# Optimization experiments

Measured on AMD Instinct MI355X. Metric: run time of the kernel, lower is better.

The kernel has to match this reference:

```python
import jax, jax.numpy as jnp
import numpy as np


def setup_inputs() -> dict:
    key = jax.random.key(0)
    k1, k2 = jax.random.split(key)
    T, C, H, W = 32, 3, 720, 1280
    x = jax.random.normal(k1, (T, C, H, W), dtype=jnp.float32)
    # flow displacements of a few pixels, realistic optical-flow magnitudes
    flow = jax.random.normal(k2, (T - 2, 2, H, W), dtype=jnp.float32) * 4.0
    return {"x": x, "flow": flow}


def reference(x, flow):
    T, C, H, W = x.shape
    N = T - 2
    # base pixel coordinate grids (computed once, broadcast over frames)
    idx_x = jnp.arange(H, dtype=jnp.float32)[:, None]   # [H,1] -> row coord
    idx_y = jnp.arange(W, dtype=jnp.float32)[None, :]   # [1,W] -> col coord

    fwd = flow[:N]        # flow[t-1] for t=1..N
    bwd = flow[::-1][:N]  # flow[-t]  for t=1..N

    # round+clamp flow-shifted coordinates (jnp.round = round-half-even, matches torch.round)
    ix_f = jnp.clip(jnp.round(idx_x + fwd[:, 0]), 0, H - 1).astype(jnp.int32)  # [N,H,W]
    iy_f = jnp.clip(jnp.round(idx_y + fwd[:, 1]), 0, W - 1).astype(jnp.int32)
    ix_b = jnp.clip(jnp.round(idx_x + bwd[:, 0]), 0, H - 1).astype(jnp.int32)
    iy_b = jnp.clip(jnp.round(idx_y + bwd[:, 1]), 0, W - 1).astype(jnp.int32)

    def gather(frame, ix, iy):  # frame [C,H,W], ix/iy [H,W] -> [C,H,W]
        return frame[:, ix, iy]

    x_fwd = jax.vmap(gather)(x[2:T], ix_f, iy_f)   # warp of x[t+1]
    x_bwd = jax.vmap(gather)(x[0:N], ix_b, iy_b)   # warp of x[t-1]
    xc = x[1:N + 1]                                # center frames x[t]

    # [N, 2C, H, W]
    return jnp.concatenate([xc - x_fwd, xc - x_bwd], axis=1)
```

## Files before the change

kernel.cpp:

```cpp
#include <hip/hip_runtime.h>
#include <hip/hip_bf16.h>


#define TT 32
#define CC 3
#define HH 720
#define WW 1280
#define NN (TT - 2)

__device__ __forceinline__ int clampi(int v, int lo, int hi) {
    return v < lo ? lo : (v > hi ? hi : v);
}

__global__ __launch_bounds__(256) void warp_diff_kernel(
    const float* __restrict__ x,
    const float* __restrict__ flow,
    float* __restrict__ out)
{
    const int WQ = WW / 4;
    int idx = blockIdx.x * blockDim.x + threadIdx.x;
    const int total = NN * HH * WQ;
    if (idx >= total) return;

    int wq = idx % WQ;
    int t  = idx / WQ;
    int h  = t % HH;
    int n  = t / HH;
    int w0 = wq * 4;

    const size_t HW = (size_t)HH * WW;
    const size_t rowoff = (size_t)h * WW + w0;

    const float4 fdx = *(const float4*)(flow + ((size_t)n * 2 + 0) * HW + rowoff);
    const float4 fdy = *(const float4*)(flow + ((size_t)n * 2 + 1) * HW + rowoff);
    const float4 bdx = *(const float4*)(flow + ((size_t)(NN - 1 - n) * 2 + 0) * HW + rowoff);
    const float4 bdy = *(const float4*)(flow + ((size_t)(NN - 1 - n) * 2 + 1) * HW + rowoff);

    float fh = (float)h;
    int ixf[4], iyf[4], ixb[4], iyb[4];
    {
        const float fdxv[4] = {fdx.x, fdx.y, fdx.z, fdx.w};
        const float fdyv[4] = {fdy.x, fdy.y, fdy.z, fdy.w};
        const float bdxv[4] = {bdx.x, bdx.y, bdx.z, bdx.w};
        const float bdyv[4] = {bdy.x, bdy.y, bdy.z, bdy.w};
#pragma unroll
        for (int j = 0; j < 4; ++j) {
            float fw = (float)(w0 + j);
            ixf[j] = clampi((int)rintf(fh + fdxv[j]), 0, HH - 1);
            iyf[j] = clampi((int)rintf(fw + fdyv[j]), 0, WW - 1);
            ixb[j] = clampi((int)rintf(fh + bdxv[j]), 0, HH - 1);
            iyb[j] = clampi((int)rintf(fw + bdyv[j]), 0, WW - 1);
        }
    }

    size_t gf[4], gb[4];
#pragma unroll
    for (int j = 0; j < 4; ++j) {
        gf[j] = (size_t)ixf[j] * WW + iyf[j];
        gb[j] = (size_t)ixb[j] * WW + iyb[j];
    }

    const float* xc_base = x + ((size_t)(n + 1) * CC) * HW + rowoff;
    const float* xf_base = x + ((size_t)(n + 2) * CC) * HW;
    const float* xb_base = x + ((size_t)(n + 0) * CC) * HW;
    float* out_f = out + ((size_t)n * 6) * HW + rowoff;
    float* out_b = out_f + 3 * HW;

#pragma unroll
    for (int c = 0; c < CC; ++c) {
        const float4 vc = *(const float4*)(xc_base + (size_t)c * HW);
        const float* xf = xf_base + (size_t)c * HW;
        const float* xb = xb_base + (size_t)c * HW;

        float4 of, ob;
        of.x = vc.x - xf[gf[0]];
        of.y = vc.y - xf[gf[1]];
        of.z = vc.z - xf[gf[2]];
        of.w = vc.w - xf[gf[3]];
        ob.x = vc.x - xb[gb[0]];
        ob.y = vc.y - xb[gb[1]];
        ob.z = vc.z - xb[gb[2]];
        ob.w = vc.w - xb[gb[3]];

        *(float4*)(out_f + (size_t)c * HW) = of;
        *(float4*)(out_b + (size_t)c * HW) = ob;
    }
}

extern "C" void kernel_launch(void* const* d_in, const int* in_sizes, int n_in,
                              void* d_out, int out_size, void* d_ws, size_t ws_size,
                              hipStream_t stream) {
    const float* x    = (const float*)d_in[0];
    const float* flow = (const float*)d_in[1];
    float* out = (float*)d_out;

    const int WQ = WW / 4;
    const int total = NN * HH * WQ;
    const int block = 256;
    const int grid = (total + block - 1) / block;
    warp_diff_kernel<<<grid, block, 0, stream>>>(x, flow, out);
}
```

Baseline: 1.603 ms.

## Tile threads into 2D blocks with XCD-aware workgroup remapping for gather locality

Each 256-thread block now covers a 16-row by 64-column tile instead of a 1D strip of one row, so the data-dependent gathers from neighbouring frames hit a compact 2D region. Block IDs are remapped so that consecutive tiles land on the same XCD, the aim being to share L2 across neighbouring tiles. Gather offsets switch from size_t to 32-bit int to cut address arithmetic. The mapping assumes dimensions divide evenly by tile sizes and NWG divides by 8, which holds here.

```diff
diff --git a/kernel.cpp b/kernel.cpp
--- a/kernel.cpp
+++ b/kernel.cpp
@@ -1,5 +1,4 @@
 #include <hip/hip_runtime.h>
-#include <hip/hip_bf16.h>
 
 
 #define TT 32
@@ -7,6 +6,14 @@
 #define HH 720
 #define WW 1280
 #define NN (TT - 2)
+
+#define TILE_H   16
+#define TILE_WQ  16
+#define TILES_W  (WW / (TILE_WQ * 4))
+#define TILES_H  (HH / TILE_H)
+#define TILES_PER_N (TILES_W * TILES_H)
+#define NWG      (NN * TILES_PER_N)
+#define NXCD     8
 
 __device__ __forceinline__ int clampi(int v, int lo, int hi) {
     return v < lo ? lo : (v > hi ? hi : v);
@@ -17,16 +24,19 @@
     const float* __restrict__ flow,
     float* __restrict__ out)
 {
-    const int WQ = WW / 4;
-    int idx = blockIdx.x * blockDim.x + threadIdx.x;
-    const int total = NN * HH * WQ;
-    if (idx >= total) return;
+    const int wid  = blockIdx.x;
+    const int work = (wid % NXCD) * (NWG / NXCD) + wid / NXCD;
 
-    int wq = idx % WQ;
-    int t  = idx / WQ;
-    int h  = t % HH;
-    int n  = t / HH;
-    int w0 = wq * 4;
+    const int tile = work % TILES_PER_N;
+    const int n    = work / TILES_PER_N;
+    const int tw   = tile % TILES_W;
+    const int th   = tile / TILES_W;
+
+    const int ty = threadIdx.x >> 4;
+    const int tx = threadIdx.x & 15;
+
+    const int h  = th * TILE_H + ty;
+    const int w0 = (tw * TILE_WQ + tx) * 4;
 
     const size_t HW = (size_t)HH * WW;
     const size_t rowoff = (size_t)h * WW + w0;
@@ -36,8 +46,8 @@
     const float4 bdx = *(const float4*)(flow + ((size_t)(NN - 1 - n) * 2 + 0) * HW + rowoff);
     const float4 bdy = *(const float4*)(flow + ((size_t)(NN - 1 - n) * 2 + 1) * HW + rowoff);
 
-    float fh = (float)h;
-    int ixf[4], iyf[4], ixb[4], iyb[4];
+    const float fh = (float)h;
+    int gf[4], gb[4];
     {
         const float fdxv[4] = {fdx.x, fdx.y, fdx.z, fdx.w};
         const float fdyv[4] = {fdy.x, fdy.y, fdy.z, fdy.w};
@@ -46,18 +56,13 @@
 #pragma unroll
         for (int j = 0; j < 4; ++j) {
             float fw = (float)(w0 + j);
-            ixf[j] = clampi((int)rintf(fh + fdxv[j]), 0, HH - 1);
-            iyf[j] = clampi((int)rintf(fw + fdyv[j]), 0, WW - 1);
-            ixb[j] = clampi((int)rintf(fh + bdxv[j]), 0, HH - 1);
-            iyb[j] = clampi((int)rintf(fw + bdyv[j]), 0, WW - 1);
+            int ixf = clampi((int)rintf(fh + fdxv[j]), 0, HH - 1);
+            int iyf = clampi((int)rintf(fw + fdyv[j]), 0, WW - 1);
+            int ixb = clampi((int)rintf(fh + bdxv[j]), 0, HH - 1);
+            int iyb = clampi((int)rintf(fw + bdyv[j]), 0, WW - 1);
+            gf[j] = ixf * WW + iyf;
+            gb[j] = ixb * WW + iyb;
         }
-    }
-
-    size_t gf[4], gb[4];
-#pragma unroll
-    for (int j = 0; j < 4; ++j) {
-        gf[j] = (size_t)ixf[j] * WW + iyf[j];
-        gb[j] = (size_t)ixb[j] * WW + iyb[j];
     }
 
     const float* xc_base = x + ((size_t)(n + 1) * CC) * HW + rowoff;
@@ -94,9 +99,5 @@
     const float* flow = (const float*)d_in[1];
     float* out = (float*)d_out;
 
-    const int WQ = WW / 4;
-    const int total = NN * HH * WQ;
-    const int block = 256;
-    const int grid = (total + block - 1) / block;
-    warp_diff_kernel<<<grid, block, 0, stream>>>(x, flow, out);
+    warp_diff_kernel<<<NWG, 256, 0, stream>>>(x, flow, out);
 }
```

Result: faster. 1.299 ms (-19.0%).
